# Optimization experiments

Hardware: AMD Instinct MI355X
Metric: run time of the kernel (lower is better)

The kernel has to match this reference:

```python
import itertools
import jax, jax.numpy as jnp
import numpy as np

# Standard JPEG luma quantization table
Y_TABLE = np.array([
    [16, 11, 10, 16, 24, 40, 51, 61],
    [12, 12, 14, 19, 26, 58, 60, 55],
    [14, 13, 16, 24, 40, 57, 69, 56],
    [14, 17, 22, 29, 51, 87, 80, 62],
    [18, 22, 37, 56, 68, 109, 103, 77],
    [24, 35, 55, 64, 81, 104, 113, 92],
    [49, 64, 78, 87, 103, 121, 120, 101],
    [72, 92, 95, 98, 112, 100, 103, 99]], dtype=np.float32)

# Standard JPEG chroma quantization table
C_TABLE = np.full((8, 8), 99.0, dtype=np.float32)
C_TABLE[:4, :4] = np.array([[17, 18, 24, 47],
                            [18, 21, 26, 66],
                            [24, 26, 56, 99],
                            [47, 66, 99, 99]], dtype=np.float32)

# IDCT normalization and cosine basis
_a = np.array([1.0 / np.sqrt(2)] + [1.0] * 7, dtype=np.float32)
ALPHA = np.outer(_a, _a).astype(np.float32)  # (8,8)
BASIS = np.zeros((8, 8, 8, 8), dtype=np.float32)
for x, y, u, v in itertools.product(range(8), repeat=4):
    BASIS[x, y, u, v] = np.cos((2 * u + 1) * x * np.pi / 16) * np.cos((2 * v + 1) * y * np.pi / 16)

# YCbCr -> RGB
COLOR_MAT = np.array([[1.0, 0.0, 1.402],
                      [1.0, -0.344136, -0.714136],
                      [1.0, 1.772, 0.0]], dtype=np.float32).T  # (3,3)
COLOR_SHIFT = np.array([0.0, -128.0, -128.0], dtype=np.float32)


def _idct_8x8(blocks):
    # blocks: (B, N, 8, 8) -> (B, N, 8, 8)
    scaled = blocks * jnp.asarray(ALPHA)
    return 0.25 * jnp.einsum('bnxy,xyuv->bnuv', scaled, jnp.asarray(BASIS)) + 128.0


def _block_merge(patches, height, width):
    # patches: (B, height//8 * width//8, 8, 8) -> (B, height, width)
    b = patches.shape[0]
    x = patches.reshape(b, height // 8, width // 8, 8, 8)
    x = x.transpose(0, 1, 3, 2, 4)
    return x.reshape(b, height, width)


def _chroma_repeat(x, k=2):
    # exact replica of the torch repeat/view trick: (B,H,W) -> (B,kH,kW)
    b, hh, ww = x.shape
    x = jnp.tile(x[..., None], (1, 1, k, k))  # (B, H, k*W, k)
    return x.reshape(b, hh * k, ww * k)


def setup_inputs() -> dict:
    key = jax.random.key(0)
    k1, k2, k3 = jax.random.split(key, 3)
    B, h, w = 16, 1024, 1024
    y = jax.random.normal(k1, (B, (h // 8) * (w // 8), 8, 8), dtype=jnp.float32)
    cb = jax.random.normal(k2, (B, (h // 16) * (w // 16), 8, 8), dtype=jnp.float32)
    cr = jax.random.normal(k3, (B, (h // 16) * (w // 16), 8, 8), dtype=jnp.float32)
    factor = jnp.ones((), dtype=jnp.float32)
    return {"y": y, "cb": cb, "cr": cr, "factor": factor, "h": h, "w": w}


def reference(y, cb, cr, factor, h, w):
    y_tab = jnp.asarray(Y_TABLE)
    c_tab = jnp.asarray(C_TABLE)

    # dequantize -> IDCT -> merge per plane
    y_img = _block_merge(_idct_8x8(y * (y_tab * factor)), h, w)
    cb_img = _block_merge(_idct_8x8(cb * (c_tab * factor)), h // 2, w // 2)
    cr_img = _block_merge(_idct_8x8(cr * (c_tab * factor)), h // 2, w // 2)

    # chroma upsampling and stack to (B, h, w, 3)
    ycc = jnp.stack([y_img, _chroma_repeat(cb_img), _chroma_repeat(cr_img)], axis=3)

    # color conversion to RGB, (B, 3, h, w)
    rgb = jnp.einsum('bhwc,cd->bhwd', ycc + jnp.asarray(COLOR_SHIFT), jnp.asarray(COLOR_MAT))
    rgb = rgb.transpose(0, 3, 1, 2)

    return jnp.clip(rgb, 0.0, 255.0) / 255.0
```

## Files before the change

### kernel.cpp

```cpp
#include <hip/hip_runtime.h>


#define IMG_W 1024
#define IMG_HW (1024 * 1024)

typedef float v4f __attribute__((ext_vector_type(4)));

static constexpr float COS_LIT[64] = {
    1.0f,          1.0f,          1.0f,          1.0f,          1.0f,          1.0f,          1.0f,          1.0f,
    0.980785280f,  0.831469612f,  0.555570233f,  0.195090322f, -0.195090322f, -0.555570233f, -0.831469612f, -0.980785280f,
    0.923879533f,  0.382683432f, -0.382683432f, -0.923879533f, -0.923879533f, -0.382683432f,  0.382683432f,  0.923879533f,
    0.831469612f, -0.195090322f, -0.980785280f, -0.555570233f,  0.555570233f,  0.980785280f,  0.195090322f, -0.831469612f,
    0.707106781f, -0.707106781f, -0.707106781f,  0.707106781f,  0.707106781f, -0.707106781f, -0.707106781f,  0.707106781f,
    0.555570233f, -0.980785280f,  0.195090322f,  0.831469612f, -0.831469612f, -0.195090322f,  0.980785280f, -0.555570233f,
    0.382683432f, -0.923879533f,  0.923879533f, -0.382683432f, -0.382683432f,  0.923879533f, -0.923879533f,  0.382683432f,
    0.195090322f, -0.555570233f,  0.831469612f, -0.980785280f,  0.980785280f, -0.831469612f,  0.555570233f, -0.195090322f};

__constant__ float COST[64] = {
    1.0f,  0.980785280f,  0.923879533f,  0.831469612f,  0.707106781f,  0.555570233f,  0.382683432f,  0.195090322f,
    1.0f,  0.831469612f,  0.382683432f, -0.195090322f, -0.707106781f, -0.980785280f, -0.923879533f, -0.555570233f,
    1.0f,  0.555570233f, -0.382683432f, -0.980785280f, -0.707106781f,  0.195090322f,  0.923879533f,  0.831469612f,
    1.0f,  0.195090322f, -0.923879533f, -0.555570233f,  0.707106781f,  0.831469612f, -0.382683432f, -0.980785280f,
    1.0f, -0.195090322f, -0.923879533f,  0.555570233f,  0.707106781f, -0.831469612f, -0.382683432f,  0.980785280f,
    1.0f, -0.555570233f, -0.382683432f,  0.980785280f, -0.707106781f, -0.195090322f,  0.923879533f, -0.831469612f,
    1.0f, -0.831469612f,  0.382683432f,  0.195090322f, -0.707106781f,  0.980785280f, -0.923879533f,  0.555570233f,
    1.0f, -0.980785280f,  0.923879533f, -0.831469612f,  0.707106781f, -0.555570233f,  0.382683432f, -0.195090322f};

__constant__ float YTAB[64] = {
    16, 11, 10, 16, 24, 40, 51, 61,
    12, 12, 14, 19, 26, 58, 60, 55,
    14, 13, 16, 24, 40, 57, 69, 56,
    14, 17, 22, 29, 51, 87, 80, 62,
    18, 22, 37, 56, 68, 109, 103, 77,
    24, 35, 55, 64, 81, 104, 113, 92,
    49, 64, 78, 87, 103, 121, 120, 101,
    72, 92, 95, 98, 112, 100, 103, 99};

__constant__ float CTAB[64] = {
    17, 18, 24, 47, 99, 99, 99, 99,
    18, 21, 26, 66, 99, 99, 99, 99,
    24, 26, 56, 99, 99, 99, 99, 99,
    47, 66, 99, 99, 99, 99, 99, 99,
    99, 99, 99, 99, 99, 99, 99, 99,
    99, 99, 99, 99, 99, 99, 99, 99,
    99, 99, 99, 99, 99, 99, 99, 99,
    99, 99, 99, 99, 99, 99, 99, 99};

__global__ __launch_bounds__(192) void jpeg_decode_kernel(
    const float* __restrict__ yq, const float* __restrict__ cbq,
    const float* __restrict__ crq, const float* __restrict__ fac,
    float* __restrict__ out)
{
    __shared__ float t1s[3][8][68];
    __shared__ float cpx[2][8][32];

    const int t   = threadIdx.x;
    const int w   = t >> 6;
    const int l   = t & 63;
    const int blk = l >> 3;
    const int row = l & 7;

    const int gid = blockIdx.x;
    const int rx  = gid & 15;
    const int ry  = (gid >> 4) & 63;
    const int img = gid >> 10;

    const float factor = fac[0];

    const float* src;
    const float* qt;
    size_t base;
    if (w < 2) {
        const int nb = (ry * 2 + w) * 128 + rx * 8 + blk;
        base = ((size_t)(img * 16384 + nb) << 6) + row * 8;
        src = yq;  qt = YTAB;
    } else {
        const int nc = ry * 64 + rx * 4 + (blk & 3);
        base = ((size_t)(img * 4096 + nc) << 6) + row * 8;
        src = (blk & 4) ? crq : cbq;  qt = CTAB;
    }
    const float4 r0 = *reinterpret_cast<const float4*>(src + base);
    const float4 r1 = *reinterpret_cast<const float4*>(src + base + 4);
    const float4 q0 = *reinterpret_cast<const float4*>(qt + row * 8);
    const float4 q1 = *reinterpret_cast<const float4*>(qt + row * 8 + 4);

    const float s = 0.25f * factor * ((row == 0) ? 0.70710678118654752f : 1.0f);
    float cf[8];
    cf[0] = r0.x * (q0.x * (s * 0.70710678118654752f));
    cf[1] = r0.y * (q0.y * s);
    cf[2] = r0.z * (q0.z * s);
    cf[3] = r0.w * (q0.w * s);
    cf[4] = r1.x * (q1.x * s);
    cf[5] = r1.y * (q1.y * s);
    cf[6] = r1.z * (q1.z * s);
    cf[7] = r1.w * (q1.w * s);

    float t1[8];
#pragma unroll
    for (int v = 0; v < 8; ++v) {
        float a = cf[0];
#pragma unroll
        for (int y = 1; y < 8; ++y) a += cf[y] * COS_LIT[y * 8 + v];
        t1[v] = a;
    }
    *reinterpret_cast<float4*>(&t1s[w][row][blk * 8])     = make_float4(t1[0], t1[1], t1[2], t1[3]);
    *reinterpret_cast<float4*>(&t1s[w][row][blk * 8 + 4]) = make_float4(t1[4], t1[5], t1[6], t1[7]);

    const int r4 = l >> 4;
    const int c  = l & 15;
    float cuA[8], cuB[8];
    {
        const float4 a0 = *reinterpret_cast<const float4*>(&COST[r4 * 8]);
        const float4 a1 = *reinterpret_cast<const float4*>(&COST[r4 * 8 + 4]);
        const float4 b0 = *reinterpret_cast<const float4*>(&COST[(r4 + 4) * 8]);
        const float4 b1 = *reinterpret_cast<const float4*>(&COST[(r4 + 4) * 8 + 4]);
        cuA[0]=a0.x; cuA[1]=a0.y; cuA[2]=a0.z; cuA[3]=a0.w;
        cuA[4]=a1.x; cuA[5]=a1.y; cuA[6]=a1.z; cuA[7]=a1.w;
        cuB[0]=b0.x; cuB[1]=b0.y; cuB[2]=b0.z; cuB[3]=b0.w;
        cuB[4]=b1.x; cuB[5]=b1.y; cuB[6]=b1.z; cuB[7]=b1.w;
    }

    float pA[4] = {0.f, 0.f, 0.f, 0.f};
    float pB[4] = {0.f, 0.f, 0.f, 0.f};
#pragma unroll
    for (int x = 0; x < 8; ++x) {
        const float4 v = *reinterpret_cast<const float4*>(&t1s[w][x][c * 4]);
        pA[0] += cuA[x] * v.x; pA[1] += cuA[x] * v.y; pA[2] += cuA[x] * v.z; pA[3] += cuA[x] * v.w;
        pB[0] += cuB[x] * v.x; pB[1] += cuB[x] * v.y; pB[2] += cuB[x] * v.z; pB[3] += cuB[x] * v.w;
    }

    if (w == 2) {
        const int pl  = c >> 3;
        const int col = (c * 4) & 31;
        *reinterpret_cast<float4*>(&cpx[pl][r4][col])     = make_float4(pA[0], pA[1], pA[2], pA[3]);
        *reinterpret_cast<float4*>(&cpx[pl][r4 + 4][col]) = make_float4(pB[0], pB[1], pB[2], pB[3]);
    }
    __syncthreads();
    if (w == 2) return;

    const int crA = w * 4 + (r4 >> 1);
    const int crB = crA + 2;
    const float2 cbA = *reinterpret_cast<const float2*>(&cpx[0][crA][c * 2]);
    const float2 crA2 = *reinterpret_cast<const float2*>(&cpx[1][crA][c * 2]);
    const float2 cbB = *reinterpret_cast<const float2*>(&cpx[0][crB][c * 2]);
    const float2 crB2 = *reinterpret_cast<const float2*>(&cpx[1][crB][c * 2]);

    const int gyA = (ry * 2 + w) * 8 + r4;
    const int gx  = rx * 64 + c * 4;
    float* o = out + (size_t)img * 3 * IMG_HW + (size_t)gyA * IMG_W + gx;

    auto convert4 = [&](const float p[4], float2 cb2, float2 cr2, float* dst) {
        float R[4], G[4], Bv[4];
#pragma unroll
        for (int j = 0; j < 4; ++j) {
            const float yv = p[j] + 128.0f;
            const float cb = (j < 2) ? cb2.x : cb2.y;
            const float cr = (j < 2) ? cr2.x : cr2.y;
            R[j]  = yv + 1.402f * cr;
            G[j]  = yv - 0.344136f * cb - 0.714136f * cr;
            Bv[j] = yv + 1.772f * cb;
        }
#pragma unroll
        for (int j = 0; j < 4; ++j) {
            R[j]  = fminf(fmaxf(R[j],  0.f), 255.f) * (1.0f / 255.0f);
            G[j]  = fminf(fmaxf(G[j],  0.f), 255.f) * (1.0f / 255.0f);
            Bv[j] = fminf(fmaxf(Bv[j], 0.f), 255.f) * (1.0f / 255.0f);
        }
        v4f rv = {R[0], R[1], R[2], R[3]};
        v4f gv = {G[0], G[1], G[2], G[3]};
        v4f bv = {Bv[0], Bv[1], Bv[2], Bv[3]};
        __builtin_nontemporal_store(rv, reinterpret_cast<v4f*>(dst));
        __builtin_nontemporal_store(gv, reinterpret_cast<v4f*>(dst + IMG_HW));
        __builtin_nontemporal_store(bv, reinterpret_cast<v4f*>(dst + 2 * IMG_HW));
    };
    convert4(pA, cbA, crA2, o);
    convert4(pB, cbB, crB2, o + 4 * IMG_W);
}

extern "C" void kernel_launch(void* const* d_in, const int* in_sizes, int n_in,
                              void* d_out, int out_size, void* d_ws, size_t ws_size,
                              hipStream_t stream) {
    const float* yq  = (const float*)d_in[0];
    const float* cbq = (const float*)d_in[1];
    const float* crq = (const float*)d_in[2];
    const float* fac = (const float*)d_in[3];
    float* out = (float*)d_out;

    const int B = in_sizes[0] / (16384 * 64);

    dim3 grid(1024 * B);
    hipLaunchKernelGGL(jpeg_decode_kernel, grid, dim3(192), 0, stream,
                       yq, cbq, crq, fac, out);
}
```

Measured before the change: 49.48 us.

## Enlarge tile to 16x256 pixels and split color-plane output across warps

Each block now decodes a 16x256 pixel region with 384 threads (six wavefronts: four luma, one Cb, one Cr) instead of 16x64 with 192 threads. Each lane handles two block rows, so it does twice the IDCT work with more registers. The full 2D IDCT result is written back to shared memory, and the color conversion is reassigned so each wavefront writes one output plane. This gives each wavefront a run of 1 KB-wide contiguous row stores per plane instead of three scattered planes. The aim is better write coalescing and fewer blocks, traded against higher register and LDS use per block and fewer blocks overall.

```diff
diff --git a/kernel.cpp b/kernel.cpp
--- a/kernel.cpp
+++ b/kernel.cpp
@@ -3,6 +3,7 @@
 
 #define IMG_W 1024
 #define IMG_HW (1024 * 1024)
+#define RSQRT2 0.70710678118654752f
 
 typedef float v4f __attribute__((ext_vector_type(4)));
 
@@ -46,135 +47,154 @@
     99, 99, 99, 99, 99, 99, 99, 99,
     99, 99, 99, 99, 99, 99, 99, 99};
 
-__global__ __launch_bounds__(192) void jpeg_decode_kernel(
+__global__ __launch_bounds__(384) void jpeg_decode_kernel(
     const float* __restrict__ yq, const float* __restrict__ cbq,
     const float* __restrict__ crq, const float* __restrict__ fac,
     float* __restrict__ out)
 {
-    __shared__ float t1s[3][8][68];
-    __shared__ float cpx[2][8][32];
+    __shared__ float sl[6][8][132];
 
     const int t   = threadIdx.x;
     const int w   = t >> 6;
     const int l   = t & 63;
-    const int blk = l >> 3;
-    const int row = l & 7;
+    const int sub = l >> 2;
+    const int r   = l & 3;
 
     const int gid = blockIdx.x;
-    const int rx  = gid & 15;
-    const int ry  = (gid >> 4) & 63;
-    const int img = gid >> 10;
+    const int rx  = gid & 3;
+    const int ry  = (gid >> 2) & 63;
+    const int img = gid >> 8;
 
     const float factor = fac[0];
 
     const float* src;
     const float* qt;
     size_t base;
-    if (w < 2) {
-        const int nb = (ry * 2 + w) * 128 + rx * 8 + blk;
-        base = ((size_t)(img * 16384 + nb) << 6) + row * 8;
+    if (w < 4) {
+        const int br = ry * 2 + (w >> 1);
+        const int bc = rx * 32 + (w & 1) * 16 + sub;
+        base = ((size_t)(img * 16384 + br * 128 + bc) << 6) + r * 8;
         src = yq;  qt = YTAB;
     } else {
-        const int nc = ry * 64 + rx * 4 + (blk & 3);
-        base = ((size_t)(img * 4096 + nc) << 6) + row * 8;
-        src = (blk & 4) ? crq : cbq;  qt = CTAB;
-    }
-    const float4 r0 = *reinterpret_cast<const float4*>(src + base);
-    const float4 r1 = *reinterpret_cast<const float4*>(src + base + 4);
-    const float4 q0 = *reinterpret_cast<const float4*>(qt + row * 8);
-    const float4 q1 = *reinterpret_cast<const float4*>(qt + row * 8 + 4);
-
-    const float s = 0.25f * factor * ((row == 0) ? 0.70710678118654752f : 1.0f);
-    float cf[8];
-    cf[0] = r0.x * (q0.x * (s * 0.70710678118654752f));
-    cf[1] = r0.y * (q0.y * s);
-    cf[2] = r0.z * (q0.z * s);
-    cf[3] = r0.w * (q0.w * s);
-    cf[4] = r1.x * (q1.x * s);
-    cf[5] = r1.y * (q1.y * s);
-    cf[6] = r1.z * (q1.z * s);
-    cf[7] = r1.w * (q1.w * s);
-
-    float t1[8];
+        base = ((size_t)(img * 4096 + ry * 64 + rx * 16 + sub) << 6) + r * 8;
+        src = (w == 5) ? crq : cbq;  qt = CTAB;
+    }
+    const float4 a0  = *reinterpret_cast<const float4*>(src + base);
+    const float4 a1  = *reinterpret_cast<const float4*>(src + base + 4);
+    const float4 b0  = *reinterpret_cast<const float4*>(src + base + 32);
+    const float4 b1  = *reinterpret_cast<const float4*>(src + base + 36);
+    const float4 qa0 = *reinterpret_cast<const float4*>(qt + r * 8);
+    const float4 qa1 = *reinterpret_cast<const float4*>(qt + r * 8 + 4);
+    const float4 qb0 = *reinterpret_cast<const float4*>(qt + (r + 4) * 8);
+    const float4 qb1 = *reinterpret_cast<const float4*>(qt + (r + 4) * 8 + 4);
+
+    const float slo = 0.25f * factor * ((r == 0) ? RSQRT2 : 1.0f);
+    const float shi = 0.25f * factor;
+    float cl[8], ch[8];
+    cl[0] = a0.x * (qa0.x * (slo * RSQRT2));
+    cl[1] = a0.y * (qa0.y * slo);
+    cl[2] = a0.z * (qa0.z * slo);
+    cl[3] = a0.w * (qa0.w * slo);
+    cl[4] = a1.x * (qa1.x * slo);
+    cl[5] = a1.y * (qa1.y * slo);
+    cl[6] = a1.z * (qa1.z * slo);
+    cl[7] = a1.w * (qa1.w * slo);
+    ch[0] = b0.x * (qb0.x * (shi * RSQRT2));
+    ch[1] = b0.y * (qb0.y * shi);
+    ch[2] = b0.z * (qb0.z * shi);
+    ch[3] = b0.w * (qb0.w * shi);
+    ch[4] = b1.x * (qb1.x * shi);
+    ch[5] = b1.y * (qb1.y * shi);
+    ch[6] = b1.z * (qb1.z * shi);
+    ch[7] = b1.w * (qb1.w * shi);
+
+    float tl[8], th[8];
 #pragma unroll
     for (int v = 0; v < 8; ++v) {
-        float a = cf[0];
-#pragma unroll
-        for (int y = 1; y < 8; ++y) a += cf[y] * COS_LIT[y * 8 + v];
-        t1[v] = a;
-    }
-    *reinterpret_cast<float4*>(&t1s[w][row][blk * 8])     = make_float4(t1[0], t1[1], t1[2], t1[3]);
-    *reinterpret_cast<float4*>(&t1s[w][row][blk * 8 + 4]) = make_float4(t1[4], t1[5], t1[6], t1[7]);
-
-    const int r4 = l >> 4;
-    const int c  = l & 15;
-    float cuA[8], cuB[8];
+        float al = cl[0], ah = ch[0];
+#pragma unroll
+        for (int y = 1; y < 8; ++y) {
+            al += cl[y] * COS_LIT[y * 8 + v];
+            ah += ch[y] * COS_LIT[y * 8 + v];
+        }
+        tl[v] = al;  th[v] = ah;
+    }
+    const int col0 = sub * 8;
+    *reinterpret_cast<float4*>(&sl[w][r][col0])         = make_float4(tl[0], tl[1], tl[2], tl[3]);
+    *reinterpret_cast<float4*>(&sl[w][r][col0 + 4])     = make_float4(tl[4], tl[5], tl[6], tl[7]);
+    *reinterpret_cast<float4*>(&sl[w][r + 4][col0])     = make_float4(th[0], th[1], th[2], th[3]);
+    *reinterpret_cast<float4*>(&sl[w][r + 4][col0 + 4]) = make_float4(th[4], th[5], th[6], th[7]);
+
+    const int rr = l >> 4;
+    const int c8 = (l & 15) * 8;
+    float cuL[8], cuH[8];
     {
-        const float4 a0 = *reinterpret_cast<const float4*>(&COST[r4 * 8]);
-        const float4 a1 = *reinterpret_cast<const float4*>(&COST[r4 * 8 + 4]);
-        const float4 b0 = *reinterpret_cast<const float4*>(&COST[(r4 + 4) * 8]);
-        const float4 b1 = *reinterpret_cast<const float4*>(&COST[(r4 + 4) * 8 + 4]);
-        cuA[0]=a0.x; cuA[1]=a0.y; cuA[2]=a0.z; cuA[3]=a0.w;
-        cuA[4]=a1.x; cuA[5]=a1.y; cuA[6]=a1.z; cuA[7]=a1.w;
-        cuB[0]=b0.x; cuB[1]=b0.y; cuB[2]=b0.z; cuB[3]=b0.w;
-        cuB[4]=b1.x; cuB[5]=b1.y; cuB[6]=b1.z; cuB[7]=b1.w;
-    }
-
-    float pA[4] = {0.f, 0.f, 0.f, 0.f};
-    float pB[4] = {0.f, 0.f, 0.f, 0.f};
+        const float4 u0 = *reinterpret_cast<const float4*>(&COST[rr * 8]);
+        const float4 u1 = *reinterpret_cast<const float4*>(&COST[rr * 8 + 4]);
+        const float4 v0 = *reinterpret_cast<const float4*>(&COST[(rr + 4) * 8]);
+        const float4 v1 = *reinterpret_cast<const float4*>(&COST[(rr + 4) * 8 + 4]);
+        cuL[0]=u0.x; cuL[1]=u0.y; cuL[2]=u0.z; cuL[3]=u0.w;
+        cuL[4]=u1.x; cuL[5]=u1.y; cuL[6]=u1.z; cuL[7]=u1.w;
+        cuH[0]=v0.x; cuH[1]=v0.y; cuH[2]=v0.z; cuH[3]=v0.w;
+        cuH[4]=v1.x; cuH[5]=v1.y; cuH[6]=v1.z; cuH[7]=v1.w;
+    }
+    float pl[8] = {0,0,0,0,0,0,0,0};
+    float ph[8] = {0,0,0,0,0,0,0,0};
 #pragma unroll
     for (int x = 0; x < 8; ++x) {
-        const float4 v = *reinterpret_cast<const float4*>(&t1s[w][x][c * 4]);
-        pA[0] += cuA[x] * v.x; pA[1] += cuA[x] * v.y; pA[2] += cuA[x] * v.z; pA[3] += cuA[x] * v.w;
-        pB[0] += cuB[x] * v.x; pB[1] += cuB[x] * v.y; pB[2] += cuB[x] * v.z; pB[3] += cuB[x] * v.w;
-    }
-
-    if (w == 2) {
-        const int pl  = c >> 3;
-        const int col = (c * 4) & 31;
-        *reinterpret_cast<float4*>(&cpx[pl][r4][col])     = make_float4(pA[0], pA[1], pA[2], pA[3]);
-        *reinterpret_cast<float4*>(&cpx[pl][r4 + 4][col]) = make_float4(pB[0], pB[1], pB[2], pB[3]);
-    }
+        const float4 va = *reinterpret_cast<const float4*>(&sl[w][x][c8]);
+        const float4 vb = *reinterpret_cast<const float4*>(&sl[w][x][c8 + 4]);
+        pl[0] += cuL[x] * va.x; pl[1] += cuL[x] * va.y; pl[2] += cuL[x] * va.z; pl[3] += cuL[x] * va.w;
+        pl[4] += cuL[x] * vb.x; pl[5] += cuL[x] * vb.y; pl[6] += cuL[x] * vb.z; pl[7] += cuL[x] * vb.w;
+        ph[0] += cuH[x] * va.x; ph[1] += cuH[x] * va.y; ph[2] += cuH[x] * va.z; ph[3] += cuH[x] * va.w;
+        ph[4] += cuH[x] * vb.x; ph[5] += cuH[x] * vb.y; ph[6] += cuH[x] * vb.z; ph[7] += cuH[x] * vb.w;
+    }
+    *reinterpret_cast<float4*>(&sl[w][rr][c8])         = make_float4(pl[0], pl[1], pl[2], pl[3]);
+    *reinterpret_cast<float4*>(&sl[w][rr][c8 + 4])     = make_float4(pl[4], pl[5], pl[6], pl[7]);
+    *reinterpret_cast<float4*>(&sl[w][rr + 4][c8])     = make_float4(ph[0], ph[1], ph[2], ph[3]);
+    *reinterpret_cast<float4*>(&sl[w][rr + 4][c8 + 4]) = make_float4(ph[4], ph[5], ph[6], ph[7]);
+
     __syncthreads();
-    if (w == 2) return;
-
-    const int crA = w * 4 + (r4 >> 1);
-    const int crB = crA + 2;
-    const float2 cbA = *reinterpret_cast<const float2*>(&cpx[0][crA][c * 2]);
-    const float2 crA2 = *reinterpret_cast<const float2*>(&cpx[1][crA][c * 2]);
-    const float2 cbB = *reinterpret_cast<const float2*>(&cpx[0][crB][c * 2]);
-    const float2 crB2 = *reinterpret_cast<const float2*>(&cpx[1][crB][c * 2]);
-
-    const int gyA = (ry * 2 + w) * 8 + r4;
-    const int gx  = rx * 64 + c * 4;
-    float* o = out + (size_t)img * 3 * IMG_HW + (size_t)gyA * IMG_W + gx;
-
-    auto convert4 = [&](const float p[4], float2 cb2, float2 cr2, float* dst) {
-        float R[4], G[4], Bv[4];
-#pragma unroll
-        for (int j = 0; j < 4; ++j) {
-            const float yv = p[j] + 128.0f;
-            const float cb = (j < 2) ? cb2.x : cb2.y;
-            const float cr = (j < 2) ? cr2.x : cr2.y;
-            R[j]  = yv + 1.402f * cr;
-            G[j]  = yv - 0.344136f * cb - 0.714136f * cr;
-            Bv[j] = yv + 1.772f * cb;
+
+    const int plane = w >> 1;
+    const int rbase = (w & 1) * 8;
+    float* const ob = out + (size_t)img * 3 * IMG_HW + (size_t)plane * IMG_HW
+                    + (size_t)(ry * 16) * IMG_W + rx * 256 + l * 4;
+
+#pragma unroll
+    for (int s2 = 0; s2 < 8; ++s2) {
+        const int rr2 = rbase + s2;
+        const int ws  = ((rr2 >> 3) << 1) + (l >> 5);
+        const float4 y4 = *reinterpret_cast<const float4*>(&sl[ws][rr2 & 7][(l & 31) * 4]);
+        const int crow = rr2 >> 1;
+        const float yv[4] = {y4.x + 128.f, y4.y + 128.f, y4.z + 128.f, y4.w + 128.f};
+        float o4[4];
+        if (plane == 0) {
+            const float2 cr2 = *reinterpret_cast<const float2*>(&sl[5][crow][l * 2]);
+            o4[0] = yv[0] + 1.402f * cr2.x;
+            o4[1] = yv[1] + 1.402f * cr2.x;
+            o4[2] = yv[2] + 1.402f * cr2.y;
+            o4[3] = yv[3] + 1.402f * cr2.y;
+        } else if (plane == 1) {
+            const float2 cb2 = *reinterpret_cast<const float2*>(&sl[4][crow][l * 2]);
+            const float2 cr2 = *reinterpret_cast<const float2*>(&sl[5][crow][l * 2]);
+            o4[0] = yv[0] - 0.344136f * cb2.x - 0.714136f * cr2.x;
+            o4[1] = yv[1] - 0.344136f * cb2.x - 0.714136f * cr2.x;
+            o4[2] = yv[2] - 0.344136f * cb2.y - 0.714136f * cr2.y;
+            o4[3] = yv[3] - 0.344136f * cb2.y - 0.714136f * cr2.y;
+        } else {
+            const float2 cb2 = *reinterpret_cast<const float2*>(&sl[4][crow][l * 2]);
+            o4[0] = yv[0] + 1.772f * cb2.x;
+            o4[1] = yv[1] + 1.772f * cb2.x;
+            o4[2] = yv[2] + 1.772f * cb2.y;
+            o4[3] = yv[3] + 1.772f * cb2.y;
         }
-#pragma unroll
-        for (int j = 0; j < 4; ++j) {
-            R[j]  = fminf(fmaxf(R[j],  0.f), 255.f) * (1.0f / 255.0f);
-            G[j]  = fminf(fmaxf(G[j],  0.f), 255.f) * (1.0f / 255.0f);
-            Bv[j] = fminf(fmaxf(Bv[j], 0.f), 255.f) * (1.0f / 255.0f);
-        }
-        v4f rv = {R[0], R[1], R[2], R[3]};
-        v4f gv = {G[0], G[1], G[2], G[3]};
-        v4f bv = {Bv[0], Bv[1], Bv[2], Bv[3]};
-        __builtin_nontemporal_store(rv, reinterpret_cast<v4f*>(dst));
-        __builtin_nontemporal_store(gv, reinterpret_cast<v4f*>(dst + IMG_HW));
-        __builtin_nontemporal_store(bv, reinterpret_cast<v4f*>(dst + 2 * IMG_HW));
-    };
-    convert4(pA, cbA, crA2, o);
-    convert4(pB, cbB, crB2, o + 4 * IMG_W);
+        v4f v;
+#pragma unroll
+        for (int j = 0; j < 4; ++j)
+            v[j] = fminf(fmaxf(o4[j], 0.f), 255.f) * (1.0f / 255.0f);
+        __builtin_nontemporal_store(v, reinterpret_cast<v4f*>(ob + (size_t)rr2 * IMG_W));
+    }
 }
 
 extern "C" void kernel_launch(void* const* d_in, const int* in_sizes, int n_in,
@@ -188,7 +208,7 @@
 
     const int B = in_sizes[0] / (16384 * 64);
 
-    dim3 grid(1024 * B);
-    hipLaunchKernelGGL(jpeg_decode_kernel, grid, dim3(192), 0, stream,
+    dim3 grid(256 * B);
+    hipLaunchKernelGGL(jpeg_decode_kernel, grid, dim3(384), 0, stream,
                        yq, cbq, crq, fac, out);
 }
```

After: 51.43 us. +3.9%, slower.
